# Kernel tuning notes

Hardware: AMD Instinct MI355X
Metric: run time of the kernel (lower is better)

Reference implementation:

```python
import jax, jax.numpy as jnp
import numpy as np

E, TOPK, D, F, FS = 16, 4, 2560, 1664, 3328
B, S = 1, 2048


def setup_inputs() -> dict:
    key = jax.random.key(0)
    ks = jax.random.split(key, 8)
    sc = lambda *sh: 1.0 / np.sqrt(sh[-2] if len(sh) > 1 else 1.0)
    return {
        "hidden_states": jax.random.normal(ks[0], (B, S, D), jnp.float32),
        "router_weight": jax.random.normal(ks[1], (E, D), jnp.float32) * (1.0 / np.sqrt(D)),
        "w_gate": jax.random.normal(ks[2], (E, D, F), jnp.float32) * (1.0 / np.sqrt(D)),
        "w_up": jax.random.normal(ks[3], (E, D, F), jnp.float32) * (1.0 / np.sqrt(D)),
        "w_down": jax.random.normal(ks[4], (E, F, D), jnp.float32) * (1.0 / np.sqrt(F)),
        "sw_gate": jax.random.normal(ks[5], (D, FS), jnp.float32) * (1.0 / np.sqrt(D)),
        "sw_up": jax.random.normal(ks[6], (D, FS), jnp.float32) * (1.0 / np.sqrt(D)),
        "sw_down": jax.random.normal(ks[7], (FS, D), jnp.float32) * (1.0 / np.sqrt(FS)),
    }


def reference(hidden_states, router_weight, w_gate, w_up, w_down, sw_gate, sw_up, sw_down):
    b, s, d = hidden_states.shape
    x = hidden_states.reshape(-1, d)  # [T, D]
    T = x.shape[0]

    # Router: linear -> softmax -> top-k -> renormalize (vLLM FusedMoE default)
    logits = x @ router_weight.T                      # [T, E]
    probs = jax.nn.softmax(logits, axis=-1)
    topk_w, topk_idx = jax.lax.top_k(probs, TOPK)     # [T, K]
    topk_w = topk_w / jnp.sum(topk_w, axis=-1, keepdims=True)
    combine = jnp.zeros((T, E), x.dtype).at[jnp.arange(T)[:, None], topk_idx].add(topk_w)  # [T, E]

    # Expert SiLU-gated MLPs (dense-dispatch reference for grouped GEMM)
    g = jnp.einsum('td,edf->tef', x, w_gate)          # [T, E, F]
    u = jnp.einsum('td,edf->tef', x, w_up)
    h = jax.nn.silu(g) * u
    y = jnp.einsum('tef,efd->ted', h, w_down)         # [T, E, D]
    sparse_out = jnp.einsum('ted,te->td', y, combine)

    # Shared expert: LlamaMLP with silu gate, no bias
    shared_out = (jax.nn.silu(x @ sw_gate) * (x @ sw_up)) @ sw_down

    return (sparse_out + shared_out).reshape(b, s, d)
```

## Files before the change

kernel.cpp:

```cpp
#include <hip/hip_runtime.h>
#include <hip/hip_bf16.h>
#include <stdint.h>

#define E_N 16
#define TOPK 4
#define DD 2560
#define FF 1664
#define FSS 3328
#define TT 2048

#define BM 128
#define BN 128
#define BK 32

typedef __attribute__((ext_vector_type(8))) __bf16 bf16x8;
typedef __attribute__((ext_vector_type(4))) float f32x4;

__device__ __forceinline__ unsigned short f2bf(float f) {
  return __builtin_bit_cast(unsigned short, (__bf16)f);
}
__device__ __forceinline__ unsigned int pk2(float a, float b) {
  return (unsigned int)f2bf(a) | ((unsigned int)f2bf(b) << 16);
}

#define GLOAD16(g, l)                                                          \
  __builtin_amdgcn_global_load_lds(                                            \
      (const __attribute__((address_space(1))) void*)(g),                      \
      (__attribute__((address_space(3))) void*)(l), 16, 0, 0)

#define SBAR() __builtin_amdgcn_s_barrier()
#define SCHED0() __builtin_amdgcn_sched_barrier(0)
#define VMW(N) asm volatile("s_waitcnt vmcnt(" #N ")" ::: "memory")

__device__ __forceinline__ void swz_block(int& bm, int& bn, int& bz) {
  int gx = gridDim.x, gy = gridDim.y;
  int nwg = gx * gy * gridDim.z;
  int flat = blockIdx.x + gx * (blockIdx.y + gy * blockIdx.z);
  if ((nwg & 7) == 0) flat = (flat & 7) * (nwg >> 3) + (flat >> 3);
  bm = flat % gx;
  int rest = flat / gx;
  bn = rest % gy;
  bz = rest / gy;
}

__global__ __launch_bounds__(256) void cvt_bf16_kernel(const float* __restrict__ in,
                                                       unsigned short* __restrict__ out) {
  size_t i = ((size_t)blockIdx.x * 256 + threadIdx.x) * 4;
  float4 v = *reinterpret_cast<const float4*>(in + i);
  ushort4 o;
  o.x = f2bf(v.x); o.y = f2bf(v.y); o.z = f2bf(v.z); o.w = f2bf(v.w);
  *reinterpret_cast<ushort4*>(out + i) = o;
}

__global__ __launch_bounds__(256) void tcvt_kernel(const float* __restrict__ in,
                                                   unsigned short* __restrict__ out,
                                                   int K, int N) {
  __shared__ float lds[64 * 65];
  int z = blockIdx.z;
  in += (size_t)z * K * N;
  out += (size_t)z * K * N;
  int k0 = blockIdx.x * 64, n0 = blockIdx.y * 64;
  int t = threadIdx.x;
#pragma unroll
  for (int j = 0; j < 4; ++j) {
    int idx = j * 256 + t;
    int r = idx >> 4, c = (idx & 15) * 4;
    float4 v = *reinterpret_cast<const float4*>(in + (size_t)(k0 + r) * N + n0 + c);
    lds[r * 65 + c] = v.x;
    lds[r * 65 + c + 1] = v.y;
    lds[r * 65 + c + 2] = v.z;
    lds[r * 65 + c + 3] = v.w;
  }
  __syncthreads();
#pragma unroll
  for (int j = 0; j < 2; ++j) {
    int idx = j * 256 + t;
    int n = idx >> 3, kg = (idx & 7) * 8;
    float a0 = lds[(kg + 0) * 65 + n], a1 = lds[(kg + 1) * 65 + n];
    float a2 = lds[(kg + 2) * 65 + n], a3 = lds[(kg + 3) * 65 + n];
    float a4 = lds[(kg + 4) * 65 + n], a5 = lds[(kg + 5) * 65 + n];
    float a6 = lds[(kg + 6) * 65 + n], a7 = lds[(kg + 7) * 65 + n];
    uint4 o{pk2(a0, a1), pk2(a2, a3), pk2(a4, a5), pk2(a6, a7)};
    *reinterpret_cast<uint4*>(out + (size_t)(n0 + n) * K + k0 + kg) = o;
  }
}

__global__ __launch_bounds__(256) void router_kernel(const float* __restrict__ x,
                                                     const float* __restrict__ rw,
                                                     int* __restrict__ cnt,
                                                     int* __restrict__ list,
                                                     float* __restrict__ tw) {
  int t = blockIdx.x;
  const float* xr = x + (size_t)t * DD;
  __shared__ float logits[E_N];
  int lane = threadIdx.x & 63, wid = threadIdx.x >> 6;
  for (int ee = 0; ee < 4; ++ee) {
    int e = wid * 4 + ee;
    const float* wr = rw + (size_t)e * DD;
    float p = 0.f;
    for (int d = lane; d < DD; d += 64) p += xr[d] * wr[d];
#pragma unroll
    for (int off = 32; off > 0; off >>= 1) p += __shfl_down(p, off);
    if (lane == 0) logits[e] = p;
  }
  __syncthreads();
  if (threadIdx.x == 0) {
    float mx = -1e30f;
    for (int e = 0; e < E_N; ++e) mx = fmaxf(mx, logits[e]);
    float pe[E_N];
    for (int e = 0; e < E_N; ++e) pe[e] = __expf(logits[e] - mx);
    int idx[TOPK]; float val[TOPK]; float s4 = 0.f;
    unsigned used = 0;
    for (int k = 0; k < TOPK; ++k) {
      int bi = 0; float bv = -1.f;
      for (int e = 0; e < E_N; ++e)
        if (!((used >> e) & 1) && pe[e] > bv) { bv = pe[e]; bi = e; }
      used |= 1u << bi; idx[k] = bi; val[k] = bv; s4 += bv;
    }
    float inv = 1.f / s4;
    for (int k = 0; k < TOPK; ++k) {
      int e2 = idx[k];
      int pos = atomicAdd(&cnt[e2], 1);
      list[e2 * TT + pos] = t * 4 + k;
      tw[t * 4 + k] = val[k] * inv;
    }
  }
}

__global__ __launch_bounds__(256, 2) void gu_kernel(
    const unsigned short* __restrict__ Xb,
    const unsigned short* __restrict__ WgT,
    const unsigned short* __restrict__ WuT,
    unsigned short* __restrict__ H,
    const int* __restrict__ list, const int* __restrict__ cnt,
    int Ktot, int Ntot, int Mfixed) {
  int bm, bn, e;
  swz_block(bm, bn, e);
  int M = cnt ? cnt[e] : Mfixed;
  int m0 = bm * BM;
  if (m0 >= M) return;
  int n0 = bn * BN;
  const unsigned short* Bg0 = WgT + (size_t)e * Ktot * Ntot;
  const unsigned short* Bu0 = WuT + (size_t)e * Ktot * Ntot;
  const int* lst = list ? (list + e * TT) : nullptr;

  __shared__ __align__(16) unsigned short lds[3][12288];

  int tid = threadIdx.x, lane = tid & 63, w = tid >> 6;

  const unsigned short* pA[2];
#pragma unroll
  for (int q = 0; q < 2; ++q) {
    int J = w * 2 + q;
    int row = J * 16 + (lane >> 2);
    int c = lane & 3;
    int cs = c ^ ((row >> 1) & 3);
    int ar = min(m0 + row, M - 1);
    int tok = lst ? (lst[ar] >> 2) : ar;
    pA[q] = Xb + (size_t)tok * Ktot + cs * 8;
  }
  const unsigned short* pGU[4];
#pragma unroll
  for (int q = 0; q < 4; ++q) {
    int J = w * 4 + q;
    int row = J * 8 + (lane >> 3);
    int c = lane & 7;
    int sc = c ^ (row & 7);
    pGU[q] = (sc < 4) ? (Bg0 + (size_t)(n0 + row) * Ktot + sc * 8)
                      : (Bu0 + (size_t)(n0 + row) * Ktot + (sc - 4) * 8);
  }

  auto issue = [&](int kt, int buf) {
    int koff = kt * BK;
    unsigned short* dA = &lds[buf][0];
    unsigned short* dGU = &lds[buf][4096];
#pragma unroll
    for (int q = 0; q < 2; ++q)
      GLOAD16(pA[q] + koff, dA + (w * 2 + q) * 512);
#pragma unroll
    for (int q = 0; q < 4; ++q)
      GLOAD16(pGU[q] + koff, dGU + (w * 4 + q) * 512);
  };

  int wr = (w >> 1) * 64, wc = (w & 1) * 64;
  int cg = lane >> 4;
  int aoff[4], goff[4], uoff[4];
#pragma unroll
  for (int m = 0; m < 4; ++m) {
    int r = wr + m * 16 + (lane & 15);
    aoff[m] = r * 32 + ((cg ^ ((r >> 1) & 3)) * 8);
  }
#pragma unroll
  for (int n = 0; n < 4; ++n) {
    int r = wc + n * 16 + (lane & 15);
    goff[n] = r * 64 + ((cg ^ (r & 7)) * 8);
    uoff[n] = r * 64 + (((cg + 4) ^ (r & 7)) * 8);
  }

  f32x4 accG[4][4] = {};
  f32x4 accU[4][4] = {};

  auto compute = [&](int buf) {
    const unsigned short* A = &lds[buf][0];
    const unsigned short* GU = &lds[buf][4096];
    bf16x8 a[4], g[4], u[4];
#pragma unroll
    for (int m = 0; m < 4; ++m)
      a[m] = __builtin_bit_cast(bf16x8, *reinterpret_cast<const uint4*>(A + aoff[m]));
#pragma unroll
    for (int n = 0; n < 4; ++n) {
      g[n] = __builtin_bit_cast(bf16x8, *reinterpret_cast<const uint4*>(GU + goff[n]));
      u[n] = __builtin_bit_cast(bf16x8, *reinterpret_cast<const uint4*>(GU + uoff[n]));
    }
    __builtin_amdgcn_s_setprio(1);
#pragma unroll
    for (int m = 0; m < 4; ++m)
#pragma unroll
      for (int n = 0; n < 4; ++n) {
        accG[m][n] = __builtin_amdgcn_mfma_f32_16x16x32_bf16(a[m], g[n], accG[m][n], 0, 0, 0);
        accU[m][n] = __builtin_amdgcn_mfma_f32_16x16x32_bf16(a[m], u[n], accU[m][n], 0, 0, 0);
      }
    __builtin_amdgcn_s_setprio(0);
  };

  int nk = Ktot / BK;
  issue(0, 0);
  issue(1, 1);
  for (int kt = 0; kt < nk; ++kt) {
    if (kt == nk - 1) { VMW(0); } else { VMW(6); }
    SCHED0();
    SBAR(); SCHED0();
    if (kt + 2 < nk) { issue(kt + 2, (kt + 2) % 3); SCHED0(); }
    compute(kt % 3);
    SCHED0();
  }

#pragma unroll
  for (int m = 0; m < 4; ++m) {
#pragma unroll
    for (int r = 0; r < 4; ++r) {
      int lr = wr + m * 16 + (lane >> 4) * 4 + r;
      int grow = m0 + lr;
      if (grow < M) {
        int code = lst ? lst[grow] : grow;
        unsigned short* Hp = H + (size_t)code * Ntot + n0 + wc + (lane & 15);
#pragma unroll
        for (int n = 0; n < 4; ++n) {
          float gg = accG[m][n][r], uu = accU[m][n][r];
          Hp[n * 16] = f2bf((gg / (1.f + __expf(-gg))) * uu);
        }
      }
    }
  }
}

__global__ __launch_bounds__(256, 3) void dn_kernel(
    const unsigned short* __restrict__ Hb,
    const unsigned short* __restrict__ WT,
    float* __restrict__ Y,
    const int* __restrict__ list, const int* __restrict__ cnt,
    const float* __restrict__ tw, int Ktot, int Ntot, int Mfixed) {
  int bm, bn, e;
  swz_block(bm, bn, e);
  int M = cnt ? cnt[e] : Mfixed;
  int m0 = bm * BM;
  if (m0 >= M) return;
  int n0 = bn * BN;
  const unsigned short* B0 = WT + (size_t)e * Ktot * Ntot;
  const int* lst = list ? (list + e * TT) : nullptr;

  __shared__ __align__(16) unsigned short lds[3][8192];

  int tid = threadIdx.x, lane = tid & 63, w = tid >> 6;

  const unsigned short* pAB[4];
#pragma unroll
  for (int q = 0; q < 4; ++q) {
    int J = w * 4 + q;
    int row = J * 8 + (lane >> 3);
    int c = lane & 7;
    int sc = c ^ (row & 7);
    if (sc < 4) {
      int ar = min(m0 + row, M - 1);
      int code = lst ? lst[ar] : ar;
      pAB[q] = Hb + (size_t)code * Ktot + sc * 8;
    } else {
      pAB[q] = B0 + (size_t)(n0 + row) * Ktot + (sc - 4) * 8;
    }
  }

  auto issue = [&](int kt, int buf) {
    int koff = kt * BK;
    unsigned short* d = &lds[buf][0];
#pragma unroll
    for (int q = 0; q < 4; ++q)
      GLOAD16(pAB[q] + koff, d + (w * 4 + q) * 512);
  };

  int wr = (w >> 1) * 64, wc = (w & 1) * 64;
  int cg = lane >> 4;
  int aoff[4], boff[4];
#pragma unroll
  for (int m = 0; m < 4; ++m) {
    int r = wr + m * 16 + (lane & 15);
    aoff[m] = r * 64 + ((cg ^ (r & 7)) * 8);
  }
#pragma unroll
  for (int n = 0; n < 4; ++n) {
    int r = wc + n * 16 + (lane & 15);
    boff[n] = r * 64 + (((cg + 4) ^ (r & 7)) * 8);
  }

  f32x4 acc[4][4] = {};

  auto compute = [&](int buf) {
    const unsigned short* AB = &lds[buf][0];
    bf16x8 a[4], b[4];
#pragma unroll
    for (int m = 0; m < 4; ++m)
      a[m] = __builtin_bit_cast(bf16x8, *reinterpret_cast<const uint4*>(AB + aoff[m]));
#pragma unroll
    for (int n = 0; n < 4; ++n)
      b[n] = __builtin_bit_cast(bf16x8, *reinterpret_cast<const uint4*>(AB + boff[n]));
    __builtin_amdgcn_s_setprio(1);
#pragma unroll
    for (int m = 0; m < 4; ++m)
#pragma unroll
      for (int n = 0; n < 4; ++n)
        acc[m][n] = __builtin_amdgcn_mfma_f32_16x16x32_bf16(a[m], b[n], acc[m][n], 0, 0, 0);
    __builtin_amdgcn_s_setprio(0);
  };

  int nk = Ktot / BK;
  issue(0, 0);
  issue(1, 1);
  for (int kt = 0; kt < nk; ++kt) {
    if (kt == nk - 1) { VMW(0); } else { VMW(4); }
    SCHED0();
    SBAR(); SCHED0();
    if (kt + 2 < nk) { issue(kt + 2, (kt + 2) % 3); SCHED0(); }
    compute(kt % 3);
    SCHED0();
  }

#pragma unroll
  for (int m = 0; m < 4; ++m) {
#pragma unroll
    for (int r = 0; r < 4; ++r) {
      int lr = wr + m * 16 + (lane >> 4) * 4 + r;
      int grow = m0 + lr;
      if (grow < M) {
        int code = lst ? lst[grow] : grow;
        float scale = tw ? tw[code] : 1.f;
        float* Yp = Y + (size_t)code * Ntot + n0 + wc + (lane & 15);
#pragma unroll
        for (int n = 0; n < 4; ++n) Yp[n * 16] = acc[m][n][r] * scale;
      }
    }
  }
}

__global__ __launch_bounds__(256) void combine_kernel(const float* __restrict__ Y,
                                                      const float* __restrict__ Ys,
                                                      float* __restrict__ out) {
  size_t i = ((size_t)blockIdx.x * 256 + threadIdx.x) * 4;
  size_t t = i / DD;
  int d = (int)(i % DD);
  float4 a = *reinterpret_cast<const float4*>(Ys + i);
#pragma unroll
  for (int k = 0; k < 4; ++k) {
    float4 v = *reinterpret_cast<const float4*>(Y + (t * 4 + k) * (size_t)DD + d);
    a.x += v.x; a.y += v.y; a.z += v.z; a.w += v.w;
  }
  *reinterpret_cast<float4*>(out + i) = a;
}

extern "C" void kernel_launch(void* const* d_in, const int* in_sizes, int n_in,
                              void* d_out, int out_size, void* d_ws, size_t ws_size,
                              hipStream_t stream) {
  const float* x  = (const float*)d_in[0];
  const float* rw = (const float*)d_in[1];
  const float* wg = (const float*)d_in[2];
  const float* wu = (const float*)d_in[3];
  const float* wd = (const float*)d_in[4];
  const float* sg = (const float*)d_in[5];
  const float* su = (const float*)d_in[6];
  const float* sd = (const float*)d_in[7];
  float* out = (float*)d_out;

  char* ws = (char*)d_ws;
  size_t off = 0;
  auto alloc = [&](size_t bytes) {
    off = (off + 255) & ~(size_t)255;
    void* p = ws + off;
    off += bytes;
    return p;
  };
  unsigned short* W1 = (unsigned short*)alloc((size_t)E_N * FF * DD * 2);
  unsigned short* W2 = (unsigned short*)alloc((size_t)E_N * FF * DD * 2);
  unsigned short* W3 = (unsigned short*)alloc((size_t)FSS * DD * 2);
  unsigned short* W4 = (unsigned short*)alloc((size_t)FSS * DD * 2);
  unsigned short* Xb = (unsigned short*)alloc((size_t)TT * DD * 2);
  unsigned short* Hx = (unsigned short*)alloc((size_t)4 * TT * FF * 2);
  unsigned short* Hs = (unsigned short*)alloc((size_t)TT * FSS * 2);
  float* Y  = (float*)alloc((size_t)4 * TT * DD * 4);
  float* Ys = (float*)alloc((size_t)TT * DD * 4);
  float* tw = (float*)alloc((size_t)4 * TT * 4);
  int* cnt  = (int*)alloc(E_N * 4);
  int* list = (int*)alloc((size_t)E_N * TT * 4);
  (void)ws_size; (void)in_sizes; (void)n_in; (void)out_size;

  hipMemsetAsync(cnt, 0, E_N * 4, stream);
  cvt_bf16_kernel<<<TT * DD / 4 / 256, 256, 0, stream>>>(x, Xb);
  router_kernel<<<TT, 256, 0, stream>>>(x, rw, cnt, list, tw);

  tcvt_kernel<<<dim3(DD / 64, FF / 64, E_N), 256, 0, stream>>>(wg, W1, DD, FF);
  tcvt_kernel<<<dim3(DD / 64, FF / 64, E_N), 256, 0, stream>>>(wu, W2, DD, FF);
  tcvt_kernel<<<dim3(DD / 64, FSS / 64, 1), 256, 0, stream>>>(sg, W3, DD, FSS);
  tcvt_kernel<<<dim3(DD / 64, FSS / 64, 1), 256, 0, stream>>>(su, W4, DD, FSS);

  gu_kernel<<<dim3(TT / BM, FF / BN, E_N), 256, 0, stream>>>(
      Xb, W1, W2, Hx, list, cnt, DD, FF, 0);
  gu_kernel<<<dim3(TT / BM, FSS / BN, 1), 256, 0, stream>>>(
      Xb, W3, W4, Hs, nullptr, nullptr, DD, FSS, TT);

  tcvt_kernel<<<dim3(FF / 64, DD / 64, E_N), 256, 0, stream>>>(wd, W1, FF, DD);
  tcvt_kernel<<<dim3(FSS / 64, DD / 64, 1), 256, 0, stream>>>(sd, W2, FSS, DD);

  dn_kernel<<<dim3(TT / BM, DD / BN, E_N), 256, 0, stream>>>(
      Hx, W1, Y, list, cnt, tw, FF, DD, 0);
  dn_kernel<<<dim3(TT / BM, DD / BN, 1), 256, 0, stream>>>(
      Hs, W2, Ys, nullptr, nullptr, nullptr, FSS, DD, TT);

  combine_kernel<<<TT * DD / 4 / 256, 256, 0, stream>>>(Y, Ys, out);
}
```

Measured before the change: 1.021 ms.

## Merge launches into three phase kernels with concurrent weight conversion

Fuses the conversion, router and transpose kernels into one launch, merges the expert and shared gate/up GEMMs with the down-projection weight transposes into a second launch, and merges both down GEMMs into a third. The aim is to cut launch gaps and tail idle time by letting independent work share one grid. Separate W5/W6 buffers are added so the down weight transposes can run alongside the gate/up GEMMs, and Y/Ys reuse the W1/W2 space. Phase 2 now runs the lightweight transpose blocks under the GEMM's 73 KB LDS allocation and 2-per-CU launch bound, which may lower their occupancy.

New measurement: 1.334 ms. 1.31x slower.

```diff
diff --git a/kernel.cpp b/kernel.cpp
--- a/kernel.cpp
+++ b/kernel.cpp
@@ -8,9 +8,6 @@
 #define FF 1664
 #define FSS 3328
 #define TT 2048
-
-#define BM 128
-#define BN 128
 #define BK 32
 
 typedef __attribute__((ext_vector_type(8))) __bf16 bf16x8;
@@ -32,34 +29,28 @@
 #define SCHED0() __builtin_amdgcn_sched_barrier(0)
 #define VMW(N) asm volatile("s_waitcnt vmcnt(" #N ")" ::: "memory")
 
-__device__ __forceinline__ void swz_block(int& bm, int& bn, int& bz) {
-  int gx = gridDim.x, gy = gridDim.y;
-  int nwg = gx * gy * gridDim.z;
-  int flat = blockIdx.x + gx * (blockIdx.y + gy * blockIdx.z);
-  if ((nwg & 7) == 0) flat = (flat & 7) * (nwg >> 3) + (flat >> 3);
-  bm = flat % gx;
-  int rest = flat / gx;
-  bn = rest % gy;
-  bz = rest / gy;
-}
-
-__global__ __launch_bounds__(256) void cvt_bf16_kernel(const float* __restrict__ in,
-                                                       unsigned short* __restrict__ out) {
-  size_t i = ((size_t)blockIdx.x * 256 + threadIdx.x) * 4;
-  float4 v = *reinterpret_cast<const float4*>(in + i);
-  ushort4 o;
-  o.x = f2bf(v.x); o.y = f2bf(v.y); o.z = f2bf(v.z); o.w = f2bf(v.w);
-  *reinterpret_cast<ushort4*>(out + i) = o;
-}
-
-__global__ __launch_bounds__(256) void tcvt_kernel(const float* __restrict__ in,
-                                                   unsigned short* __restrict__ out,
-                                                   int K, int N) {
-  __shared__ float lds[64 * 65];
-  int z = blockIdx.z;
-  in += (size_t)z * K * N;
-  out += (size_t)z * K * N;
-  int k0 = blockIdx.x * 64, n0 = blockIdx.y * 64;
+#define NB_TGW 16640
+#define NB_TGU 16640
+#define NB_TSG 2080
+#define NB_TSU 2080
+#define NB_CVT 5120
+#define NB_RTR 2048
+#define NB_P1 (NB_TGW + NB_TGU + NB_TSG + NB_TSU + NB_CVT + NB_RTR)
+
+#define NB_GUE 3328
+#define NB_GUS 416
+#define NB_GU (NB_GUE + NB_GUS)
+#define NB_TWD 16640
+#define NB_TSD 2080
+#define NB_P2 (NB_GU + NB_TWD + NB_TSD)
+
+#define NB_DNE 5120
+#define NB_DNS 320
+#define NB_DN (NB_DNE + NB_DNS)
+
+__device__ __forceinline__ void tcvt_body(const float* __restrict__ in,
+                                          unsigned short* __restrict__ out,
+                                          int K, int N, int k0, int n0, float* lds) {
   int t = threadIdx.x;
 #pragma unroll
   for (int j = 0; j < 4; ++j) {
@@ -85,67 +76,95 @@
   }
 }
 
-__global__ __launch_bounds__(256) void router_kernel(const float* __restrict__ x,
-                                                     const float* __restrict__ rw,
-                                                     int* __restrict__ cnt,
-                                                     int* __restrict__ list,
-                                                     float* __restrict__ tw) {
-  int t = blockIdx.x;
-  const float* xr = x + (size_t)t * DD;
-  __shared__ float logits[E_N];
-  int lane = threadIdx.x & 63, wid = threadIdx.x >> 6;
-  for (int ee = 0; ee < 4; ++ee) {
-    int e = wid * 4 + ee;
-    const float* wr = rw + (size_t)e * DD;
-    float p = 0.f;
-    for (int d = lane; d < DD; d += 64) p += xr[d] * wr[d];
-#pragma unroll
-    for (int off = 32; off > 0; off >>= 1) p += __shfl_down(p, off);
-    if (lane == 0) logits[e] = p;
-  }
-  __syncthreads();
-  if (threadIdx.x == 0) {
-    float mx = -1e30f;
-    for (int e = 0; e < E_N; ++e) mx = fmaxf(mx, logits[e]);
-    float pe[E_N];
-    for (int e = 0; e < E_N; ++e) pe[e] = __expf(logits[e] - mx);
-    int idx[TOPK]; float val[TOPK]; float s4 = 0.f;
-    unsigned used = 0;
-    for (int k = 0; k < TOPK; ++k) {
-      int bi = 0; float bv = -1.f;
-      for (int e = 0; e < E_N; ++e)
-        if (!((used >> e) & 1) && pe[e] > bv) { bv = pe[e]; bi = e; }
-      used |= 1u << bi; idx[k] = bi; val[k] = bv; s4 += bv;
-    }
-    float inv = 1.f / s4;
-    for (int k = 0; k < TOPK; ++k) {
-      int e2 = idx[k];
-      int pos = atomicAdd(&cnt[e2], 1);
-      list[e2 * TT + pos] = t * 4 + k;
-      tw[t * 4 + k] = val[k] * inv;
-    }
-  }
-}
-
-__global__ __launch_bounds__(256, 2) void gu_kernel(
+__global__ __launch_bounds__(256) void phase1_kernel(
+    const float* __restrict__ x, const float* __restrict__ rw,
+    const float* __restrict__ wg, const float* __restrict__ wu,
+    const float* __restrict__ sg, const float* __restrict__ su,
+    unsigned short* __restrict__ Xb,
+    unsigned short* __restrict__ W1, unsigned short* __restrict__ W2,
+    unsigned short* __restrict__ W3, unsigned short* __restrict__ W4,
+    int* __restrict__ cnt, int* __restrict__ list, float* __restrict__ tw) {
+  __shared__ __align__(16) unsigned char smem[16640];
+  int b = blockIdx.x;
+  if (b < NB_TGW) {
+    int z = b / 1040, r = b % 1040, bx = r % 40, by = r / 40;
+    tcvt_body(wg + (size_t)z * DD * FF, W1 + (size_t)z * DD * FF, DD, FF,
+              bx * 64, by * 64, (float*)smem);
+    return;
+  }
+  b -= NB_TGW;
+  if (b < NB_TGU) {
+    int z = b / 1040, r = b % 1040, bx = r % 40, by = r / 40;
+    tcvt_body(wu + (size_t)z * DD * FF, W2 + (size_t)z * DD * FF, DD, FF,
+              bx * 64, by * 64, (float*)smem);
+    return;
+  }
+  b -= NB_TGU;
+  if (b < NB_TSG) {
+    int bx = b % 40, by = b / 40;
+    tcvt_body(sg, W3, DD, FSS, bx * 64, by * 64, (float*)smem);
+    return;
+  }
+  b -= NB_TSG;
+  if (b < NB_TSU) {
+    int bx = b % 40, by = b / 40;
+    tcvt_body(su, W4, DD, FSS, bx * 64, by * 64, (float*)smem);
+    return;
+  }
+  b -= NB_TSU;
+  if (b < NB_CVT) {
+    size_t i = ((size_t)b * 256 + threadIdx.x) * 4;
+    float4 v = *reinterpret_cast<const float4*>(x + i);
+    ushort4 o;
+    o.x = f2bf(v.x); o.y = f2bf(v.y); o.z = f2bf(v.z); o.w = f2bf(v.w);
+    *reinterpret_cast<ushort4*>(Xb + i) = o;
+    return;
+  }
+  b -= NB_CVT;
+  {
+    int t = b;
+    const float* xr = x + (size_t)t * DD;
+    float* logits = (float*)smem;
+    int lane = threadIdx.x & 63, wid = threadIdx.x >> 6;
+    for (int ee = 0; ee < 4; ++ee) {
+      int e = wid * 4 + ee;
+      const float* wr = rw + (size_t)e * DD;
+      float p = 0.f;
+      for (int d = lane; d < DD; d += 64) p += xr[d] * wr[d];
+#pragma unroll
+      for (int off = 32; off > 0; off >>= 1) p += __shfl_down(p, off);
+      if (lane == 0) logits[e] = p;
+    }
+    __syncthreads();
+    if (threadIdx.x == 0) {
+      float mx = -1e30f;
+      for (int e = 0; e < E_N; ++e) mx = fmaxf(mx, logits[e]);
+      float pe[E_N];
+      for (int e = 0; e < E_N; ++e) pe[e] = __expf(logits[e] - mx);
+      int idx[TOPK]; float val[TOPK]; float s4 = 0.f;
+      unsigned used = 0;
+      for (int k = 0; k < TOPK; ++k) {
+        int bi = 0; float bv = -1.f;
+        for (int e = 0; e < E_N; ++e)
+          if (!((used >> e) & 1) && pe[e] > bv) { bv = pe[e]; bi = e; }
+        used |= 1u << bi; idx[k] = bi; val[k] = bv; s4 += bv;
+      }
+      float inv = 1.f / s4;
+      for (int k = 0; k < TOPK; ++k) {
+        int e2 = idx[k];
+        int pos = atomicAdd(&cnt[e2], 1);
+        list[e2 * TT + pos] = t * 4 + k;
+        tw[t * 4 + k] = val[k] * inv;
+      }
+    }
+  }
+}
+
+__device__ __forceinline__ void gu_body(
     const unsigned short* __restrict__ Xb,
-    const unsigned short* __restrict__ WgT,
-    const unsigned short* __restrict__ WuT,
-    unsigned short* __restrict__ H,
-    const int* __restrict__ list, const int* __restrict__ cnt,
-    int Ktot, int Ntot, int Mfixed) {
-  int bm, bn, e;
-  swz_block(bm, bn, e);
-  int M = cnt ? cnt[e] : Mfixed;
-  int m0 = bm * BM;
-  if (m0 >= M) return;
-  int n0 = bn * BN;
-  const unsigned short* Bg0 = WgT + (size_t)e * Ktot * Ntot;
-  const unsigned short* Bu0 = WuT + (size_t)e * Ktot * Ntot;
-  const int* lst = list ? (list + e * TT) : nullptr;
-
-  __shared__ __align__(16) unsigned short lds[3][12288];
-
+    const unsigned short* __restrict__ Bg0, const unsigned short* __restrict__ Bu0,
+    unsigned short* __restrict__ H, const int* lst,
+    int M, int Ktot, int Ntot, int m0, int n0, unsigned short* ldsbase) {
   int tid = threadIdx.x, lane = tid & 63, w = tid >> 6;
 
   const unsigned short* pA[2];
@@ -172,8 +191,8 @@
 
   auto issue = [&](int kt, int buf) {
     int koff = kt * BK;
-    unsigned short* dA = &lds[buf][0];
-    unsigned short* dGU = &lds[buf][4096];
+    unsigned short* dA = ldsbase + buf * 12288;
+    unsigned short* dGU = dA + 4096;
 #pragma unroll
     for (int q = 0; q < 2; ++q)
       GLOAD16(pA[q] + koff, dA + (w * 2 + q) * 512);
@@ -201,8 +220,8 @@
   f32x4 accU[4][4] = {};
 
   auto compute = [&](int buf) {
-    const unsigned short* A = &lds[buf][0];
-    const unsigned short* GU = &lds[buf][4096];
+    const unsigned short* A = ldsbase + buf * 12288;
+    const unsigned short* GU = A + 4096;
     bf16x8 a[4], g[4], u[4];
 #pragma unroll
     for (int m = 0; m < 4; ++m)
@@ -254,22 +273,77 @@
   }
 }
 
-__global__ __launch_bounds__(256, 3) void dn_kernel(
-    const unsigned short* __restrict__ Hb,
-    const unsigned short* __restrict__ WT,
-    float* __restrict__ Y,
+__global__ __launch_bounds__(256, 2) void phase2_kernel(
+    const unsigned short* __restrict__ Xb,
+    const unsigned short* __restrict__ W1, const unsigned short* __restrict__ W2,
+    const unsigned short* __restrict__ W3, const unsigned short* __restrict__ W4,
+    unsigned short* __restrict__ Hx, unsigned short* __restrict__ Hs,
     const int* __restrict__ list, const int* __restrict__ cnt,
-    const float* __restrict__ tw, int Ktot, int Ntot, int Mfixed) {
-  int bm, bn, e;
-  swz_block(bm, bn, e);
-  int M = cnt ? cnt[e] : Mfixed;
-  int m0 = bm * BM;
+    const float* __restrict__ wd, const float* __restrict__ sd,
+    unsigned short* __restrict__ W5, unsigned short* __restrict__ W6) {
+  __shared__ __align__(16) unsigned char smem[73728];
+  int b = blockIdx.x;
+  if (b < NB_GU) {
+    int swz = (b & 7) * (NB_GU / 8) + (b >> 3);
+    int bm, bn, z;
+    if (swz < NB_GUE) { z = swz / 208; int r = swz % 208; bm = r & 15; bn = r >> 4; }
+    else { int i = swz - NB_GUE; z = E_N; bm = i & 15; bn = i >> 4; }
+    const unsigned short *G0, *U0;
+    unsigned short* O0;
+    const int* lst = nullptr;
+    int M, Nt;
+    if (z < E_N) {
+      M = cnt[z]; lst = list + z * TT; Nt = FF;
+      G0 = W1 + (size_t)z * DD * FF; U0 = W2 + (size_t)z * DD * FF; O0 = Hx;
+    } else {
+      M = TT; Nt = FSS; G0 = W3; U0 = W4; O0 = Hs;
+    }
+    int m0 = bm * 128, n0 = bn * 128;
+    if (m0 >= M || n0 >= Nt) return;
+    gu_body(Xb, G0, U0, O0, lst, M, DD, Nt, m0, n0, (unsigned short*)smem);
+    return;
+  }
+  b -= NB_GU;
+  if (b < NB_TWD) {
+    int z = b / 1040, r = b % 1040, bx = r % 26, by = r / 26;
+    tcvt_body(wd + (size_t)z * FF * DD, W5 + (size_t)z * FF * DD, FF, DD,
+              bx * 64, by * 64, (float*)smem);
+    return;
+  }
+  b -= NB_TWD;
+  {
+    int bx = b % 52, by = b / 52;
+    tcvt_body(sd, W6, FSS, DD, bx * 64, by * 64, (float*)smem);
+  }
+}
+
+__global__ __launch_bounds__(256, 3) void phase3_kernel(
+    const unsigned short* __restrict__ Hx, const unsigned short* __restrict__ Hs,
+    const unsigned short* __restrict__ W5, const unsigned short* __restrict__ W6,
+    float* __restrict__ Y, float* __restrict__ Ys,
+    const int* __restrict__ list, const int* __restrict__ cnt,
+    const float* __restrict__ tw) {
+  __shared__ __align__(16) unsigned short lds[3][8192];
+  int b = blockIdx.x;
+  int swz = (b & 7) * (NB_DN / 8) + (b >> 3);
+  int bm, bn, z;
+  if (swz < NB_DNE) { z = swz / 320; int r = swz % 320; bm = r & 15; bn = r >> 4; }
+  else { int i = swz - NB_DNE; z = E_N; bm = i & 15; bn = i >> 4; }
+
+  const unsigned short* A0;
+  const unsigned short* B0;
+  float* O0;
+  const int* lst = nullptr;
+  const float* sc = nullptr;
+  int M, Kt;
+  if (z < E_N) {
+    M = cnt[z]; lst = list + z * TT; Kt = FF;
+    A0 = Hx; B0 = W5 + (size_t)z * FF * DD; O0 = Y; sc = tw;
+  } else {
+    M = TT; Kt = FSS; A0 = Hs; B0 = W6; O0 = Ys;
+  }
+  int m0 = bm * 128, n0 = bn * 128;
   if (m0 >= M) return;
-  int n0 = bn * BN;
-  const unsigned short* B0 = WT + (size_t)e * Ktot * Ntot;
-  const int* lst = list ? (list + e * TT) : nullptr;
-
-  __shared__ __align__(16) unsigned short lds[3][8192];
 
   int tid = threadIdx.x, lane = tid & 63, w = tid >> 6;
 
@@ -279,13 +353,13 @@
     int J = w * 4 + q;
     int row = J * 8 + (lane >> 3);
     int c = lane & 7;
-    int sc = c ^ (row & 7);
-    if (sc < 4) {
+    int scx = c ^ (row & 7);
+    if (scx < 4) {
       int ar = min(m0 + row, M - 1);
       int code = lst ? lst[ar] : ar;
-      pAB[q] = Hb + (size_t)code * Ktot + sc * 8;
+      pAB[q] = A0 + (size_t)code * Kt + scx * 8;
     } else {
-      pAB[q] = B0 + (size_t)(n0 + row) * Ktot + (sc - 4) * 8;
+      pAB[q] = B0 + (size_t)(n0 + row) * Kt + (scx - 4) * 8;
     }
   }
 
@@ -315,23 +389,23 @@
 
   auto compute = [&](int buf) {
     const unsigned short* AB = &lds[buf][0];
-    bf16x8 a[4], b[4];
+    bf16x8 a[4], bb[4];
 #pragma unroll
     for (int m = 0; m < 4; ++m)
       a[m] = __builtin_bit_cast(bf16x8, *reinterpret_cast<const uint4*>(AB + aoff[m]));
 #pragma unroll
     for (int n = 0; n < 4; ++n)
-      b[n] = __builtin_bit_cast(bf16x8, *reinterpret_cast<const uint4*>(AB + boff[n]));
+      bb[n] = __builtin_bit_cast(bf16x8, *reinterpret_cast<const uint4*>(AB + boff[n]));
     __builtin_amdgcn_s_setprio(1);
 #pragma unroll
     for (int m = 0; m < 4; ++m)
 #pragma unroll
       for (int n = 0; n < 4; ++n)
-        acc[m][n] = __builtin_amdgcn_mfma_f32_16x16x32_bf16(a[m], b[n], acc[m][n], 0, 0, 0);
+        acc[m][n] = __builtin_amdgcn_mfma_f32_16x16x32_bf16(a[m], bb[n], acc[m][n], 0, 0, 0);
     __builtin_amdgcn_s_setprio(0);
   };
 
-  int nk = Ktot / BK;
+  int nk = Kt / BK;
   issue(0, 0);
   issue(1, 1);
   for (int kt = 0; kt < nk; ++kt) {
@@ -351,8 +425,8 @@
       int grow = m0 + lr;
       if (grow < M) {
         int code = lst ? lst[grow] : grow;
-        float scale = tw ? tw[code] : 1.f;
-        float* Yp = Y + (size_t)code * Ntot + n0 + wc + (lane & 15);
+        float scale = sc ? sc[code] : 1.f;
+        float* Yp = O0 + (size_t)code * DD + n0 + wc + (lane & 15);
 #pragma unroll
         for (int n = 0; n < 4; ++n) Yp[n * 16] = acc[m][n][r] * scale;
       }
@@ -400,37 +474,27 @@
   unsigned short* W2 = (unsigned short*)alloc((size_t)E_N * FF * DD * 2);
   unsigned short* W3 = (unsigned short*)alloc((size_t)FSS * DD * 2);
   unsigned short* W4 = (unsigned short*)alloc((size_t)FSS * DD * 2);
+  unsigned short* W5 = (unsigned short*)alloc((size_t)E_N * FF * DD * 2);
+  unsigned short* W6 = (unsigned short*)alloc((size_t)FSS * DD * 2);
   unsigned short* Xb = (unsigned short*)alloc((size_t)TT * DD * 2);
   unsigned short* Hx = (unsigned short*)alloc((size_t)4 * TT * FF * 2);
   unsigned short* Hs = (unsigned short*)alloc((size_t)TT * FSS * 2);
-  float* Y  = (float*)alloc((size_t)4 * TT * DD * 4);
-  float* Ys = (float*)alloc((size_t)TT * DD * 4);
   float* tw = (float*)alloc((size_t)4 * TT * 4);
   int* cnt  = (int*)alloc(E_N * 4);
   int* list = (int*)alloc((size_t)E_N * TT * 4);
+  float* Y  = (float*)W2;
+  float* Ys = (float*)W1;
   (void)ws_size; (void)in_sizes; (void)n_in; (void)out_size;
 
   hipMemsetAsync(cnt, 0, E_N * 4, stream);
-  cvt_bf16_kernel<<<TT * DD / 4 / 256, 256, 0, stream>>>(x, Xb);
-  router_kernel<<<TT, 256, 0, stream>>>(x, rw, cnt, list, tw);
-
-  tcvt_kernel<<<dim3(DD / 64, FF / 64, E_N), 256, 0, stream>>>(wg, W1, DD, FF);
-  tcvt_kernel<<<dim3(DD / 64, FF / 64, E_N), 256, 0, stream>>>(wu, W2, DD, FF);
-  tcvt_kernel<<<dim3(DD / 64, FSS / 64, 1), 256, 0, stream>>>(sg, W3, DD, FSS);
-  tcvt_kernel<<<dim3(DD / 64, FSS / 64, 1), 256, 0, stream>>>(su, W4, DD, FSS);
-
-  gu_kernel<<<dim3(TT / BM, FF / BN, E_N), 256, 0, stream>>>(
-      Xb, W1, W2, Hx, list, cnt, DD, FF, 0);
-  gu_kernel<<<dim3(TT / BM, FSS / BN, 1), 256, 0, stream>>>(
-      Xb, W3, W4, Hs, nullptr, nullptr, DD, FSS, TT);
-
-  tcvt_kernel<<<dim3(FF / 64, DD / 64, E_N), 256, 0, stream>>>(wd, W1, FF, DD);
-  tcvt_kernel<<<dim3(FSS / 64, DD / 64, 1), 256, 0, stream>>>(sd, W2, FSS, DD);
-
-  dn_kernel<<<dim3(TT / BM, DD / BN, E_N), 256, 0, stream>>>(
-      Hx, W1, Y, list, cnt, tw, FF, DD, 0);
-  dn_kernel<<<dim3(TT / BM, DD / BN, 1), 256, 0, stream>>>(
-      Hs, W2, Ys, nullptr, nullptr, nullptr, FSS, DD, TT);
+
+  phase1_kernel<<<NB_P1, 256, 0, stream>>>(x, rw, wg, wu, sg, su,
+                                           Xb, W1, W2, W3, W4, cnt, list, tw);
+
+  phase2_kernel<<<NB_P2, 256, 0, stream>>>(Xb, W1, W2, W3, W4, Hx, Hs, list, cnt,
+                                           wd, sd, W5, W6);
+
+  phase3_kernel<<<NB_DN, 256, 0, stream>>>(Hx, Hs, W5, W6, Y, Ys, list, cnt, tw);
 
   combine_kernel<<<TT * DD / 4 / 256, 256, 0, stream>>>(Y, Ys, out);
 }
```
